# Performance work log

Hardware: AMD Instinct MI355X
Metric: run time of the kernel (lower is better)

The kernel has to match this reference:

```python
import jax, jax.numpy as jnp
import numpy as np

N_NODES = 10000
N_EDGES = 160000
HID = 128
N_LAYERS = 6
N_RBF = 50
CUTOFF = 10.0
EDGE_IN = 2 * HID + N_RBF + 1  # 307


def setup_inputs() -> dict:
    key = jax.random.key(0)
    ks = jax.random.split(key, 24)
    s = 0.05
    inp = {
        'atomic_numbers': jax.random.randint(ks[0], (N_NODES,), 0, 100),
        'coords': jax.random.normal(ks[1], (N_NODES, 3), jnp.float32),
        'edge_index': jax.random.randint(ks[2], (2, N_EDGES), 0, N_NODES),
        'embed': jax.random.normal(ks[3], (100, HID), jnp.float32) * s,
        # message_net (stacked over layers)
        'mw1': jax.random.normal(ks[4], (N_LAYERS, EDGE_IN, HID), jnp.float32) * s,
        'mb1': jnp.zeros((N_LAYERS, HID), jnp.float32),
        'mw2': jax.random.normal(ks[5], (N_LAYERS, HID, HID), jnp.float32) * s,
        'mb2': jnp.zeros((N_LAYERS, HID), jnp.float32),
        # coord_net
        'cw1': jax.random.normal(ks[6], (N_LAYERS, HID, HID), jnp.float32) * s,
        'cb1': jnp.zeros((N_LAYERS, HID), jnp.float32),
        'cw2': jax.random.normal(ks[7], (N_LAYERS, HID, 1), jnp.float32) * s,
        'cb2': jnp.zeros((N_LAYERS, 1), jnp.float32),
        # feature_net
        'fw': jax.random.normal(ks[8], (N_LAYERS, 2 * HID, HID), jnp.float32) * s,
        'fb': jnp.zeros((N_LAYERS, HID), jnp.float32),
        # energy_predictor
        'ew1': jax.random.normal(ks[9], (HID, HID), jnp.float32) * s,
        'eb1': jnp.zeros((HID,), jnp.float32),
        'ew2': jax.random.normal(ks[10], (HID, 1), jnp.float32) * s,
        'eb2': jnp.zeros((1,), jnp.float32),
    }
    return inp


def _forward(atomic_numbers, coords, edge_index, embed,
             mw1, mb1, mw2, mb2, cw1, cb1, cw2, cb2, fw, fb,
             ew1, eb1, ew2, eb2):
    silu = jax.nn.silu
    n = coords.shape[0]
    row, col = edge_index[0], edge_index[1]
    feats = embed[atomic_numbers]                    # [N, H]
    # RBF edge attributes (computed once from initial coords)
    d = jnp.linalg.norm(coords[row] - coords[col], axis=-1)[:, None]  # [E,1]
    centers = jnp.linspace(0.0, CUTOFF, N_RBF)
    width = CUTOFF / N_RBF
    rbf = jnp.exp(-((d - centers) ** 2) / width)
    cut = 0.5 * (jnp.cos(jnp.pi * d / CUTOFF) + 1.0) * (d < CUTOFF).astype(d.dtype)
    edge_attr = rbf * cut                            # [E, 50]
    for l in range(N_LAYERS):
        diff = coords[row] - coords[col]             # [E, 3]
        edist = jnp.sum(diff * diff, axis=-1, keepdims=True)  # squared dist, [E,1]
        ef = jnp.concatenate([feats[row], feats[col], edist, edge_attr], axis=-1)
        m = silu(silu(ef @ mw1[l] + mb1[l]) @ mw2[l] + mb2[l])        # [E, H]
        w = silu(m @ cw1[l] + cb1[l]) @ cw2[l] + cb2[l]               # [E, 1]
        coords = coords.at[row].add(w * diff)                         # equivariant coord update
        agg = jax.ops.segment_sum(m, row, num_segments=n)             # [N, H]
        feats = silu(jnp.concatenate([feats, agg], axis=-1) @ fw[l] + fb[l])
    atom_e = silu(feats @ ew1 + eb1) @ ew2 + eb2     # [N, 1]
    return jnp.sum(atom_e)


def reference(atomic_numbers, coords, edge_index, embed,
              mw1, mb1, mw2, mb2, cw1, cb1, cw2, cb2, fw, fb,
              ew1, eb1, ew2, eb2):
    return _forward(atomic_numbers, coords, edge_index, embed,
                    mw1, mb1, mw2, mb2, cw1, cb1, cw2, cb2, fw, fb,
                    ew1, eb1, ew2, eb2)
```

## Files before the change

kernel.cpp:

```cpp
#include <hip/hip_runtime.h>
#include <math.h>

#define N_NODES  10000
#define N_EDGES  160000
#define HID      128
#define N_LAYERS 6
#define N_RBF    50
#define EDGE_IN  307
#define KP1      320

typedef short bf16x8 __attribute__((ext_vector_type(8)));
typedef float f32x4  __attribute__((ext_vector_type(4)));

__device__ __forceinline__ float silu_f(float x) {
    return x / (1.0f + __expf(-x));
}
__device__ __forceinline__ short f2bf(float f) {
    union { float f; unsigned u; } v; v.f = f;
    unsigned r = v.u + 0x7FFFu + ((v.u >> 16) & 1u);
    return (short)(r >> 16);
}
__device__ __forceinline__ float bf2f(unsigned short s) {
    union { float f; unsigned u; } v; v.u = ((unsigned)s) << 16;
    return v.f;
}


__global__ void init_feats_kernel(const int* __restrict__ an,
                                  const float* __restrict__ embed,
                                  short* __restrict__ featsB) {
    int idx = blockIdx.x * blockDim.x + threadIdx.x;
    if (idx < N_NODES * HID) {
        int i = idx >> 7, j = idx & 127;
        featsB[idx] = f2bf(embed[an[i] * HID + j]);
    }
}

__global__ void hist_kernel(const int* __restrict__ row, int* __restrict__ cnt) {
    int e = blockIdx.x * blockDim.x + threadIdx.x;
    if (e < N_EDGES) atomicAdd(&cnt[row[e]], 1);
}

__global__ void scan_kernel(const int* __restrict__ cnt, int* __restrict__ cursor) {
    __shared__ int buf[256];
    __shared__ int carry;
    int tid = threadIdx.x;
    if (tid == 0) carry = 0;
    __syncthreads();
    for (int base = 0; base < N_NODES; base += 256) {
        int v = (base + tid < N_NODES) ? cnt[base + tid] : 0;
        buf[tid] = v;
        __syncthreads();
        for (int off = 1; off < 256; off <<= 1) {
            int x = (tid >= off) ? buf[tid - off] : 0;
            __syncthreads();
            buf[tid] += x;
            __syncthreads();
        }
        int excl = buf[tid] - v + carry;
        if (base + tid < N_NODES) cursor[base + tid] = excl;
        int tot = buf[255];
        __syncthreads();
        if (tid == 0) carry += tot;
        __syncthreads();
    }
}

__global__ void scatter_kernel(const int* __restrict__ row, int* __restrict__ cursor,
                               int* __restrict__ sorted) {
    int e = blockIdx.x * blockDim.x + threadIdx.x;
    if (e < N_EDGES) {
        int p = atomicAdd(&cursor[row[e]], 1);
        sorted[p] = e;
    }
}

__global__ void edgegeom_kernel(const int* __restrict__ sorted,
                                const int* __restrict__ erow, const int* __restrict__ ecol,
                                const float* __restrict__ coords,
                                float* __restrict__ d0, float* __restrict__ cut0) {
    int p = blockIdx.x * 256 + threadIdx.x;
    if (p < N_EDGES) {
        int e = sorted[p];
        int r = erow[e], c = ecol[e];
        float dx = coords[3*r]   - coords[3*c];
        float dy = coords[3*r+1] - coords[3*c+1];
        float dz = coords[3*r+2] - coords[3*c+2];
        float d = sqrtf(dx*dx + dy*dy + dz*dz);
        d0[p] = d;
        cut0[p] = (d < 10.0f) ? 0.5f * (__cosf(0.31415926535f * d) + 1.0f) : 0.0f;
    }
}

#define WT_L (40960 + 16384 + 16384 + 32768)
__global__ void wtrans_kernel(const float* __restrict__ mw1, const float* __restrict__ mw2,
                              const float* __restrict__ cw1, const float* __restrict__ fw,
                              short* __restrict__ wtm1, short* __restrict__ wtm2,
                              short* __restrict__ wtc1, short* __restrict__ wtf) {
    int idx = blockIdx.x * blockDim.x + threadIdx.x;
    if (idx >= N_LAYERS * WT_L) return;
    int l = idx / WT_L;
    int r = idx - l * WT_L;
    if (r < 40960) {
        int n = r / KP1, k = r - n * KP1;
        float v = (k < EDGE_IN) ? mw1[(size_t)l * EDGE_IN * HID + (size_t)k * HID + n] : 0.f;
        wtm1[(size_t)l * 40960 + r] = f2bf(v);
    } else if ((r -= 40960) < 16384) {
        int n = r >> 7, k = r & 127;
        wtm2[(size_t)l * 16384 + r] = f2bf(mw2[(size_t)l * HID * HID + (size_t)k * HID + n]);
    } else if ((r -= 16384) < 16384) {
        int n = r >> 7, k = r & 127;
        wtc1[(size_t)l * 16384 + r] = f2bf(cw1[(size_t)l * HID * HID + (size_t)k * HID + n]);
    } else {
        r -= 16384;
        int n = r >> 8, k = r & 255;
        wtf[(size_t)l * 32768 + r] = f2bf(fw[(size_t)l * 2 * HID * HID + (size_t)k * HID + n]);
    }
}


__global__ __launch_bounds__(256) void edge_kernel(
    const int* __restrict__ sorted,
    const int* __restrict__ erow, const int* __restrict__ ecol,
    const float* __restrict__ coords, float* __restrict__ coords_next,
    const short* __restrict__ featsB,
    const float* __restrict__ d0g, const float* __restrict__ cut0g,
    const short* __restrict__ wtm1, const float* __restrict__ mb1,
    const short* __restrict__ wtm2, const float* __restrict__ mb2,
    const short* __restrict__ wtc1, const float* __restrict__ cb1,
    const float* __restrict__ cw2, const float* __restrict__ cb2,
    float* __restrict__ agg)
{
    __shared__ short sA[64][72];
    __shared__ short sH[64][136];
    __shared__ int   srow[64];
    __shared__ int   scol[64];
    __shared__ float sdiff[64][3];
    __shared__ float sdist[64], sd0[64], scut[64], sW[64];
    __shared__ float sB1[HID], sB2[HID], sC1[HID], sV[HID];

    const int tid = threadIdx.x;
    const int p0 = blockIdx.x * 64;
    const int wave = tid >> 6, lane = tid & 63, quad = lane >> 4, lm = lane & 15;

    if (tid < 64) {
        int e = sorted[p0 + tid];
        int r = erow[e], c = ecol[e];
        srow[tid] = r; scol[tid] = c;
        float dx = coords[3*r]   - coords[3*c];
        float dy = coords[3*r+1] - coords[3*c+1];
        float dz = coords[3*r+2] - coords[3*c+2];
        sdiff[tid][0] = dx; sdiff[tid][1] = dy; sdiff[tid][2] = dz;
        sdist[tid] = dx*dx + dy*dy + dz*dz;
        sd0[tid]  = d0g[p0 + tid];
        scut[tid] = cut0g[p0 + tid];
    }
    if (tid < HID) {
        sB1[tid] = mb1[tid]; sB2[tid] = mb2[tid];
        sC1[tid] = cb1[tid]; sV[tid]  = cw2[tid];
    }
    __syncthreads();

    f32x4 acc[4][2];
    #pragma unroll
    for (int mt = 0; mt < 4; ++mt) { acc[mt][0] = (f32x4)0.f; acc[mt][1] = (f32x4)0.f; }

    for (int c = 0; c < 5; ++c) {
        int k0 = c * 64;
        {
            int el = tid >> 2, kq = (tid & 3) * 16;
            if (c < 4) {
                int node = (c < 2) ? srow[el] : scol[el];
                int off = (k0 & 127) + kq;
                const bf16x8* src = (const bf16x8*)&featsB[(size_t)node * HID + off];
                *(bf16x8*)&sA[el][kq]     = src[0];
                *(bf16x8*)&sA[el][kq + 8] = src[1];
            } else {
                float dv = sd0[el], ct = scut[el], ds2 = sdist[el];
                #pragma unroll
                for (int j = 0; j < 16; ++j) {
                    int k = 256 + kq + j;
                    float v = 0.f;
                    if (k == 256) v = ds2;
                    else if (k < EDGE_IN) {
                        float cen = (float)(k - 257) * (10.0f / 49.0f);
                        float t = dv - cen;
                        v = __expf(-t * t * 5.0f) * ct;
                    }
                    sA[el][kq + j] = f2bf(v);
                }
            }
        }
        __syncthreads();
        #pragma unroll
        for (int h = 0; h < 2; ++h) {
            bf16x8 af[4];
            #pragma unroll
            for (int mt = 0; mt < 4; ++mt)
                af[mt] = *(bf16x8*)&sA[mt * 16 + lm][h * 32 + quad * 8];
            #pragma unroll
            for (int nb = 0; nb < 2; ++nb) {
                int col = wave * 32 + nb * 16 + lm;
                bf16x8 bf = *(const bf16x8*)&wtm1[(size_t)col * KP1 + k0 + h * 32 + quad * 8];
                #pragma unroll
                for (int mt = 0; mt < 4; ++mt)
                    acc[mt][nb] = __builtin_amdgcn_mfma_f32_16x16x32_bf16(af[mt], bf, acc[mt][nb], 0, 0, 0);
            }
        }
        __syncthreads();
    }
    #pragma unroll
    for (int nb = 0; nb < 2; ++nb) {
        int col = wave * 32 + nb * 16 + lm;
        float b = sB1[col];
        #pragma unroll
        for (int mt = 0; mt < 4; ++mt) {
            #pragma unroll
            for (int r = 0; r < 4; ++r)
                sH[mt * 16 + quad * 4 + r][col] = f2bf(silu_f(acc[mt][nb][r] + b));
            acc[mt][nb] = (f32x4)0.f;
        }
    }
    __syncthreads();

    #pragma unroll
    for (int ks = 0; ks < 4; ++ks) {
        bf16x8 af[4];
        #pragma unroll
        for (int mt = 0; mt < 4; ++mt)
            af[mt] = *(bf16x8*)&sH[mt * 16 + lm][ks * 32 + quad * 8];
        #pragma unroll
        for (int nb = 0; nb < 2; ++nb) {
            int col = wave * 32 + nb * 16 + lm;
            bf16x8 bf = *(const bf16x8*)&wtm2[(size_t)col * HID + ks * 32 + quad * 8];
            #pragma unroll
            for (int mt = 0; mt < 4; ++mt)
                acc[mt][nb] = __builtin_amdgcn_mfma_f32_16x16x32_bf16(af[mt], bf, acc[mt][nb], 0, 0, 0);
        }
    }
    __syncthreads();
    #pragma unroll
    for (int nb = 0; nb < 2; ++nb) {
        int col = wave * 32 + nb * 16 + lm;
        float b = sB2[col];
        #pragma unroll
        for (int mt = 0; mt < 4; ++mt) {
            float g = 0.f;
            #pragma unroll
            for (int r = 0; r < 4; ++r) {
                int row = mt * 16 + quad * 4 + r;
                float mv = silu_f(acc[mt][nb][r] + b);
                sH[row][col] = f2bf(mv);
                g += mv;
                if (r == 3 || srow[row + 1] != srow[row]) {
                    atomicAdd(&agg[(size_t)srow[row] * HID + col], g);
                    g = 0.f;
                }
            }
            acc[mt][nb] = (f32x4)0.f;
        }
    }
    __syncthreads();

    #pragma unroll
    for (int ks = 0; ks < 4; ++ks) {
        bf16x8 af[4];
        #pragma unroll
        for (int mt = 0; mt < 4; ++mt)
            af[mt] = *(bf16x8*)&sH[mt * 16 + lm][ks * 32 + quad * 8];
        #pragma unroll
        for (int nb = 0; nb < 2; ++nb) {
            int col = wave * 32 + nb * 16 + lm;
            bf16x8 bf = *(const bf16x8*)&wtc1[(size_t)col * HID + ks * 32 + quad * 8];
            #pragma unroll
            for (int mt = 0; mt < 4; ++mt)
                acc[mt][nb] = __builtin_amdgcn_mfma_f32_16x16x32_bf16(af[mt], bf, acc[mt][nb], 0, 0, 0);
        }
    }
    __syncthreads();
    #pragma unroll
    for (int nb = 0; nb < 2; ++nb) {
        int col = wave * 32 + nb * 16 + lm;
        float b = sC1[col];
        #pragma unroll
        for (int mt = 0; mt < 4; ++mt)
            #pragma unroll
            for (int r = 0; r < 4; ++r)
                sH[mt * 16 + quad * 4 + r][col] = f2bf(silu_f(acc[mt][nb][r] + b));
    }
    __syncthreads();

    if (tid < 64) {
        float s = cb2[0];
        for (int k = 0; k < HID; k++) s += bf2f(((unsigned short*)sH[tid])[k]) * sV[k];
        sW[tid] = s;
    }
    __syncthreads();
    if (tid < 64) {
        bool leader = (tid == 0) || (srow[tid] != srow[tid - 1]);
        if (leader) {
            int rr = srow[tid];
            float ax = 0.f, ay = 0.f, az = 0.f;
            for (int k = tid; k < 64 && srow[k] == rr; ++k) {
                ax += sW[k] * sdiff[k][0];
                ay += sW[k] * sdiff[k][1];
                az += sW[k] * sdiff[k][2];
            }
            atomicAdd(&coords_next[3*rr+0], ax);
            atomicAdd(&coords_next[3*rr+1], ay);
            atomicAdd(&coords_next[3*rr+2], az);
        }
    }
}

__global__ __launch_bounds__(256) void node_kernel(
    const short* __restrict__ featsB, const float* __restrict__ agg,
    const short* __restrict__ wtf, const float* __restrict__ fb,
    short* __restrict__ outB)
{
    __shared__ short sA[32][72];
    __shared__ short sO[32][136];
    __shared__ float sFb[HID];

    const int tid = threadIdx.x;
    const int n0 = blockIdx.x * 32;
    const int wave = tid >> 6, lane = tid & 63, quad = lane >> 4, lm = lane & 15;

    if (tid < HID) sFb[tid] = fb[tid];

    f32x4 acc[2][2];
    acc[0][0] = (f32x4)0.f; acc[0][1] = (f32x4)0.f;
    acc[1][0] = (f32x4)0.f; acc[1][1] = (f32x4)0.f;
    __syncthreads();

    for (int c = 0; c < 4; ++c) {
        int k0 = c * 64;
        {
            int el = tid >> 3, kq = (tid & 7) * 8;
            int node = n0 + el;
            if (node < N_NODES) {
                if (c < 2) {
                    *(bf16x8*)&sA[el][kq] =
                        *(const bf16x8*)&featsB[(size_t)node * HID + k0 + kq];
                } else {
                    const float* ap = &agg[(size_t)node * HID + (k0 - 128) + kq];
                    bf16x8 v;
                    #pragma unroll
                    for (int j = 0; j < 8; ++j) v[j] = f2bf(ap[j]);
                    *(bf16x8*)&sA[el][kq] = v;
                }
            } else {
                *(bf16x8*)&sA[el][kq] = (bf16x8)0;
            }
        }
        __syncthreads();
        #pragma unroll
        for (int h = 0; h < 2; ++h) {
            bf16x8 af[2];
            af[0] = *(bf16x8*)&sA[lm][h * 32 + quad * 8];
            af[1] = *(bf16x8*)&sA[16 + lm][h * 32 + quad * 8];
            #pragma unroll
            for (int nb = 0; nb < 2; ++nb) {
                int col = wave * 32 + nb * 16 + lm;
                bf16x8 bf = *(const bf16x8*)&wtf[(size_t)col * 256 + k0 + h * 32 + quad * 8];
                acc[0][nb] = __builtin_amdgcn_mfma_f32_16x16x32_bf16(af[0], bf, acc[0][nb], 0, 0, 0);
                acc[1][nb] = __builtin_amdgcn_mfma_f32_16x16x32_bf16(af[1], bf, acc[1][nb], 0, 0, 0);
            }
        }
        __syncthreads();
    }
    #pragma unroll
    for (int nb = 0; nb < 2; ++nb) {
        int col = wave * 32 + nb * 16 + lm;
        float b = sFb[col];
        #pragma unroll
        for (int mt = 0; mt < 2; ++mt)
            #pragma unroll
            for (int r = 0; r < 4; ++r)
                sO[mt * 16 + quad * 4 + r][col] = f2bf(silu_f(acc[mt][nb][r] + b));
    }
    __syncthreads();
    {
        int row = tid >> 3, ch = (tid & 7) * 8;
        int hrow = row >> 1;
        (void)hrow;
        int node = n0 + row;
        if (node < N_NODES)
            *(bf16x8*)&outB[(size_t)node * HID + ch] = *(bf16x8*)&sO[row][ch];
        row += 0;
        if (node < N_NODES)
            *(bf16x8*)&outB[(size_t)node * HID + 64 + ch] = *(bf16x8*)&sO[row][64 + ch];
    }
}

#define FMA8(r, aq) \
    acc[r][0] += (aq)*b0.x; acc[r][1] += (aq)*b0.y; acc[r][2] += (aq)*b0.z; acc[r][3] += (aq)*b0.w; \
    acc[r][4] += (aq)*b1.x; acc[r][5] += (aq)*b1.y; acc[r][6] += (aq)*b1.z; acc[r][7] += (aq)*b1.w;

__global__ __launch_bounds__(256) void energy_kernel(
    const short* __restrict__ featsB,
    const float* __restrict__ ew1, const float* __restrict__ eb1,
    const float* __restrict__ ew2, const float* __restrict__ eb2,
    float* __restrict__ out)
{
    __shared__ float sA[64][20];
    __shared__ float sB[16][HID];
    __shared__ float sV[HID];
    __shared__ float red[256];
    int tid = threadIdx.x;
    int n0 = blockIdx.x * 64;
    const int tr = tid >> 4, tc = tid & 15;
    const int r0 = tr * 4, c0 = tc * 4, c1 = c0 + 64;
    const int el = tid >> 2, kq = (tid & 3) * 4;

    if (tid < HID) sV[tid] = ew2[tid];

    float acc[4][8];
    #pragma unroll
    for (int i = 0; i < 4; i++)
        #pragma unroll
        for (int j = 0; j < 8; j++) acc[i][j] = 0.f;

    for (int kt = 0; kt < 8; ++kt) {
        int k0 = kt * 16;
        {
            int k = k0 + kq;
            int node = n0 + el;
            float4 v = make_float4(0,0,0,0);
            if (node < N_NODES) {
                const unsigned short* p = (const unsigned short*)&featsB[(size_t)node * HID + k];
                v.x = bf2f(p[0]); v.y = bf2f(p[1]); v.z = bf2f(p[2]); v.w = bf2f(p[3]);
            }
            *(float4*)&sA[el][kq] = v;
        }
        {
            int bk = tid >> 4, bj = (tid & 15) * 8;
            int k = k0 + bk;
            *(float4*)&sB[bk][bj]     = *(const float4*)&ew1[(size_t)k * HID + bj];
            *(float4*)&sB[bk][bj + 4] = *(const float4*)&ew1[(size_t)k * HID + bj + 4];
        }
        __syncthreads();
        #pragma unroll
        for (int kk4 = 0; kk4 < 4; ++kk4) {
            float4 a0 = *(const float4*)&sA[r0 + 0][kk4 * 4];
            float4 a1 = *(const float4*)&sA[r0 + 1][kk4 * 4];
            float4 a2 = *(const float4*)&sA[r0 + 2][kk4 * 4];
            float4 a3 = *(const float4*)&sA[r0 + 3][kk4 * 4];
            #pragma unroll
            for (int q = 0; q < 4; ++q) {
                int kk = kk4 * 4 + q;
                float4 b0 = *(const float4*)&sB[kk][c0];
                float4 b1 = *(const float4*)&sB[kk][c1];
                float q0 = ((const float*)&a0)[q], q1 = ((const float*)&a1)[q];
                float q2 = ((const float*)&a2)[q], q3 = ((const float*)&a3)[q];
                FMA8(0, q0) FMA8(1, q1) FMA8(2, q2) FMA8(3, q3)
            }
        }
        __syncthreads();
    }
    float part = 0.f;
    #pragma unroll
    for (int i = 0; i < 4; i++) {
        int node = n0 + r0 + i;
        if (node < N_NODES) {
            #pragma unroll
            for (int j = 0; j < 4; j++) {
                part += silu_f(acc[i][j]     + eb1[c0+j]) * sV[c0+j];
                part += silu_f(acc[i][4 + j] + eb1[c1+j]) * sV[c1+j];
            }
        }
    }
    red[tid] = part;
    __syncthreads();
    for (int s = 128; s > 0; s >>= 1) {
        if (tid < s) red[tid] += red[tid + s];
        __syncthreads();
    }
    if (tid == 0) {
        float v = red[0];
        if (blockIdx.x == 0) v += eb2[0] * (float)N_NODES;
        atomicAdd(out, v);
    }
}


extern "C" void kernel_launch(void* const* d_in, const int* in_sizes, int n_in,
                              void* d_out, int out_size, void* d_ws, size_t ws_size,
                              hipStream_t stream)
{
    const int*   an     = (const int*)  d_in[0];
    const float* coords = (const float*)d_in[1];
    const int*   ei     = (const int*)  d_in[2];
    const float* embed  = (const float*)d_in[3];
    const float* mw1 = (const float*)d_in[4];
    const float* mb1 = (const float*)d_in[5];
    const float* mw2 = (const float*)d_in[6];
    const float* mb2 = (const float*)d_in[7];
    const float* cw1 = (const float*)d_in[8];
    const float* cb1 = (const float*)d_in[9];
    const float* cw2 = (const float*)d_in[10];
    const float* cb2 = (const float*)d_in[11];
    const float* fw  = (const float*)d_in[12];
    const float* fb  = (const float*)d_in[13];
    const float* ew1 = (const float*)d_in[14];
    const float* eb1 = (const float*)d_in[15];
    const float* ew2 = (const float*)d_in[16];
    const float* eb2 = (const float*)d_in[17];
    float* out = (float*)d_out;

    char* w = (char*)d_ws;
    size_t off = 0;
    auto alloc = [&](size_t bytes) -> char* {
        char* p = w + off;
        off = (off + bytes + 511) & ~(size_t)511;
        return p;
    };
    short* featsB0 = (short*)alloc((size_t)N_NODES * HID * 2);
    short* featsB1 = (short*)alloc((size_t)N_NODES * HID * 2);
    float* agg     = (float*)alloc((size_t)N_NODES * HID * 4);
    float* cA      = (float*)alloc((size_t)N_NODES * 3 * 4);
    float* cB      = (float*)alloc((size_t)N_NODES * 3 * 4);
    float* d0      = (float*)alloc((size_t)N_EDGES * 4);
    float* cut0    = (float*)alloc((size_t)N_EDGES * 4);
    int*   sorted  = (int*)  alloc((size_t)N_EDGES * 4);
    int*   cnt     = (int*)  alloc((size_t)N_NODES * 4);
    int*   cursor  = (int*)  alloc((size_t)N_NODES * 4);
    short* wtm1    = (short*)alloc((size_t)N_LAYERS * 40960 * 2);
    short* wtm2    = (short*)alloc((size_t)N_LAYERS * 16384 * 2);
    short* wtc1    = (short*)alloc((size_t)N_LAYERS * 16384 * 2);
    short* wtf     = (short*)alloc((size_t)N_LAYERS * 32768 * 2);

    const int* erow = ei;
    const int* ecol = ei + N_EDGES;

    hipMemsetAsync(cnt, 0, (size_t)N_NODES * 4, stream);
    init_feats_kernel<<<(N_NODES * HID + 255) / 256, 256, 0, stream>>>(an, embed, featsB0);
    wtrans_kernel<<<(N_LAYERS * WT_L + 255) / 256, 256, 0, stream>>>(
        mw1, mw2, cw1, fw, wtm1, wtm2, wtc1, wtf);
    hipMemcpyAsync(cA, coords, (size_t)N_NODES * 3 * 4, hipMemcpyDeviceToDevice, stream);
    hist_kernel<<<(N_EDGES + 255) / 256, 256, 0, stream>>>(erow, cnt);
    scan_kernel<<<1, 256, 0, stream>>>(cnt, cursor);
    scatter_kernel<<<(N_EDGES + 255) / 256, 256, 0, stream>>>(erow, cursor, sorted);
    edgegeom_kernel<<<N_EDGES / 256, 256, 0, stream>>>(sorted, erow, ecol, cA, d0, cut0);

    short* fc = featsB0; short* fn = featsB1;
    float* cc = cA;      float* cn = cB;
    for (int l = 0; l < N_LAYERS; ++l) {
        hipMemsetAsync(agg, 0, (size_t)N_NODES * HID * 4, stream);
        hipMemcpyAsync(cn, cc, (size_t)N_NODES * 3 * 4, hipMemcpyDeviceToDevice, stream);
        edge_kernel<<<N_EDGES / 64, 256, 0, stream>>>(
            sorted, erow, ecol, cc, cn, fc, d0, cut0,
            wtm1 + (size_t)l * 40960, mb1 + (size_t)l * HID,
            wtm2 + (size_t)l * 16384, mb2 + (size_t)l * HID,
            wtc1 + (size_t)l * 16384, cb1 + (size_t)l * HID,
            cw2 + (size_t)l * HID,    cb2 + l, agg);
        node_kernel<<<(N_NODES + 31) / 32, 256, 0, stream>>>(
            fc, agg, wtf + (size_t)l * 32768, fb + (size_t)l * HID, fn);
        { short* t = fc; fc = fn; fn = t; }
        { float* t = cc; cc = cn; cn = t; }
    }
    hipMemsetAsync(out, 0, 4, stream);
    energy_kernel<<<(N_NODES + 63) / 64, 256, 0, stream>>>(fc, ew1, eb1, ew2, eb2, out);
}
```

Baseline: 802.2 us.

## Make edge kernel persistent with register-resident weights and double-buffered gathers

The edge kernel becomes persistent: 512 blocks loop over 64-edge tiles and load all per-layer MFMA B-fragments (mw1, mw2, cw1) into registers once per block instead of once per tile. The feature gather for the next K-chunk is prefetched into registers and written to a second shared buffer while MFMAs run on the current one. The coord-net output layer is folded into the accumulator epilogue with shuffle reductions, which removes an sH round trip and a serial 128-wide dot product per edge. The trade-off is 36 bf16x8 weight registers per thread, which raises register pressure under launch_bounds(256,2), and a fixed grid size that may not match the number of CUs.

```diff
diff --git a/kernel.cpp b/kernel.cpp
--- a/kernel.cpp
+++ b/kernel.cpp
@@ -8,6 +8,8 @@
 #define N_RBF    50
 #define EDGE_IN  307
 #define KP1      320
+#define N_TILES  (N_EDGES / 64)
+#define EDGE_GRID 512
 
 typedef short bf16x8 __attribute__((ext_vector_type(8)));
 typedef float f32x4  __attribute__((ext_vector_type(4)));
@@ -119,7 +121,7 @@
 }
 
 
-__global__ __launch_bounds__(256) void edge_kernel(
+__global__ __launch_bounds__(256, 2) void edge_kernel(
     const int* __restrict__ sorted,
     const int* __restrict__ erow, const int* __restrict__ ecol,
     const float* __restrict__ coords, float* __restrict__ coords_next,
@@ -131,54 +133,85 @@
     const float* __restrict__ cw2, const float* __restrict__ cb2,
     float* __restrict__ agg)
 {
-    __shared__ short sA[64][72];
+    __shared__ short sA[2][64][72];
     __shared__ short sH[64][136];
     __shared__ int   srow[64];
     __shared__ int   scol[64];
     __shared__ float sdiff[64][3];
     __shared__ float sdist[64], sd0[64], scut[64], sW[64];
+    __shared__ float sWp[64][4];
     __shared__ float sB1[HID], sB2[HID], sC1[HID], sV[HID];
 
     const int tid = threadIdx.x;
-    const int p0 = blockIdx.x * 64;
     const int wave = tid >> 6, lane = tid & 63, quad = lane >> 4, lm = lane & 15;
-
-    if (tid < 64) {
-        int e = sorted[p0 + tid];
-        int r = erow[e], c = ecol[e];
-        srow[tid] = r; scol[tid] = c;
-        float dx = coords[3*r]   - coords[3*c];
-        float dy = coords[3*r+1] - coords[3*c+1];
-        float dz = coords[3*r+2] - coords[3*c+2];
-        sdiff[tid][0] = dx; sdiff[tid][1] = dy; sdiff[tid][2] = dz;
-        sdist[tid] = dx*dx + dy*dy + dz*dz;
-        sd0[tid]  = d0g[p0 + tid];
-        scut[tid] = cut0g[p0 + tid];
-    }
+    const int el = tid >> 2, kq = (tid & 3) * 16;
+    const int colA = wave * 32 + lm;
+    const int colB = colA + 16;
+
     if (tid < HID) {
         sB1[tid] = mb1[tid]; sB2[tid] = mb2[tid];
         sC1[tid] = cb1[tid]; sV[tid]  = cw2[tid];
     }
-    __syncthreads();
-
-    f32x4 acc[4][2];
+    bf16x8 bw1[20], bw2[8], bw3[8];
     #pragma unroll
-    for (int mt = 0; mt < 4; ++mt) { acc[mt][0] = (f32x4)0.f; acc[mt][1] = (f32x4)0.f; }
-
-    for (int c = 0; c < 5; ++c) {
-        int k0 = c * 64;
+    for (int c = 0; c < 5; ++c)
+        #pragma unroll
+        for (int h = 0; h < 2; ++h) {
+            bw1[c*4 + h*2 + 0] = *(const bf16x8*)&wtm1[(size_t)colA * KP1 + c*64 + h*32 + quad*8];
+            bw1[c*4 + h*2 + 1] = *(const bf16x8*)&wtm1[(size_t)colB * KP1 + c*64 + h*32 + quad*8];
+        }
+    #pragma unroll
+    for (int ks = 0; ks < 4; ++ks) {
+        bw2[ks*2 + 0] = *(const bf16x8*)&wtm2[(size_t)colA * HID + ks*32 + quad*8];
+        bw2[ks*2 + 1] = *(const bf16x8*)&wtm2[(size_t)colB * HID + ks*32 + quad*8];
+        bw3[ks*2 + 0] = *(const bf16x8*)&wtc1[(size_t)colA * HID + ks*32 + quad*8];
+        bw3[ks*2 + 1] = *(const bf16x8*)&wtc1[(size_t)colB * HID + ks*32 + quad*8];
+    }
+    const float cb2v = cb2[0];
+
+    for (int tile = blockIdx.x; tile < N_TILES; tile += EDGE_GRID) {
+        const int p0 = tile * 64;
+        __syncthreads();
+
+        if (tid < 64) {
+            int e = sorted[p0 + tid];
+            int r = erow[e], c = ecol[e];
+            srow[tid] = r; scol[tid] = c;
+            float dx = coords[3*r]   - coords[3*c];
+            float dy = coords[3*r+1] - coords[3*c+1];
+            float dz = coords[3*r+2] - coords[3*c+2];
+            sdiff[tid][0] = dx; sdiff[tid][1] = dy; sdiff[tid][2] = dz;
+            sdist[tid] = dx*dx + dy*dy + dz*dz;
+            sd0[tid]  = d0g[p0 + tid];
+            scut[tid] = cut0g[p0 + tid];
+        }
+        __syncthreads();
+
+        f32x4 acc[4][2];
+        #pragma unroll
+        for (int mt = 0; mt < 4; ++mt) { acc[mt][0] = (f32x4)0.f; acc[mt][1] = (f32x4)0.f; }
+
+        bf16x8 pA0, pA1;
         {
-            int el = tid >> 2, kq = (tid & 3) * 16;
-            if (c < 4) {
-                int node = (c < 2) ? srow[el] : scol[el];
-                int off = (k0 & 127) + kq;
-                const bf16x8* src = (const bf16x8*)&featsB[(size_t)node * HID + off];
-                *(bf16x8*)&sA[el][kq]     = src[0];
-                *(bf16x8*)&sA[el][kq + 8] = src[1];
-            } else {
+            int node = srow[el];
+            const bf16x8* src = (const bf16x8*)&featsB[(size_t)node * HID + kq];
+            pA0 = src[0]; pA1 = src[1];
+        }
+        *(bf16x8*)&sA[0][el][kq]     = pA0;
+        *(bf16x8*)&sA[0][el][kq + 8] = pA1;
+        __syncthreads();
+
+        #pragma unroll
+        for (int c = 0; c < 5; ++c) {
+            if (c < 3) {
+                int node = (c + 1 < 2) ? srow[el] : scol[el];
+                const bf16x8* src =
+                    (const bf16x8*)&featsB[(size_t)node * HID + ((c + 1) & 1) * 64 + kq];
+                pA0 = src[0]; pA1 = src[1];
+            } else if (c == 3) {
                 float dv = sd0[el], ct = scut[el], ds2 = sdist[el];
                 #pragma unroll
-                for (int j = 0; j < 16; ++j) {
+                for (int j = 0; j < 8; ++j) {
                     int k = 256 + kq + j;
                     float v = 0.f;
                     if (k == 256) v = ds2;
@@ -187,128 +220,147 @@
                         float t = dv - cen;
                         v = __expf(-t * t * 5.0f) * ct;
                     }
-                    sA[el][kq + j] = f2bf(v);
+                    pA0[j] = f2bf(v);
                 }
-            }
-        }
-        __syncthreads();
-        #pragma unroll
-        for (int h = 0; h < 2; ++h) {
+                #pragma unroll
+                for (int j = 0; j < 8; ++j) {
+                    int k = 264 + kq + j;
+                    float v = 0.f;
+                    if (k < EDGE_IN) {
+                        float cen = (float)(k - 257) * (10.0f / 49.0f);
+                        float t = dv - cen;
+                        v = __expf(-t * t * 5.0f) * ct;
+                    }
+                    pA1[j] = f2bf(v);
+                }
+            }
+            #pragma unroll
+            for (int h = 0; h < 2; ++h) {
+                bf16x8 af[4];
+                #pragma unroll
+                for (int mt = 0; mt < 4; ++mt)
+                    af[mt] = *(bf16x8*)&sA[c & 1][mt * 16 + lm][h * 32 + quad * 8];
+                #pragma unroll
+                for (int nb = 0; nb < 2; ++nb)
+                    #pragma unroll
+                    for (int mt = 0; mt < 4; ++mt)
+                        acc[mt][nb] = __builtin_amdgcn_mfma_f32_16x16x32_bf16(
+                            af[mt], bw1[c*4 + h*2 + nb], acc[mt][nb], 0, 0, 0);
+            }
+            if (c < 4) {
+                *(bf16x8*)&sA[(c + 1) & 1][el][kq]     = pA0;
+                *(bf16x8*)&sA[(c + 1) & 1][el][kq + 8] = pA1;
+            }
+            __syncthreads();
+        }
+        #pragma unroll
+        for (int nb = 0; nb < 2; ++nb) {
+            int col = wave * 32 + nb * 16 + lm;
+            float b = sB1[col];
+            #pragma unroll
+            for (int mt = 0; mt < 4; ++mt) {
+                #pragma unroll
+                for (int r = 0; r < 4; ++r)
+                    sH[mt * 16 + quad * 4 + r][col] = f2bf(silu_f(acc[mt][nb][r] + b));
+                acc[mt][nb] = (f32x4)0.f;
+            }
+        }
+        __syncthreads();
+
+        #pragma unroll
+        for (int ks = 0; ks < 4; ++ks) {
             bf16x8 af[4];
             #pragma unroll
             for (int mt = 0; mt < 4; ++mt)
-                af[mt] = *(bf16x8*)&sA[mt * 16 + lm][h * 32 + quad * 8];
+                af[mt] = *(bf16x8*)&sH[mt * 16 + lm][ks * 32 + quad * 8];
+            #pragma unroll
+            for (int nb = 0; nb < 2; ++nb)
+                #pragma unroll
+                for (int mt = 0; mt < 4; ++mt)
+                    acc[mt][nb] = __builtin_amdgcn_mfma_f32_16x16x32_bf16(
+                        af[mt], bw2[ks*2 + nb], acc[mt][nb], 0, 0, 0);
+        }
+        __syncthreads();
+        #pragma unroll
+        for (int nb = 0; nb < 2; ++nb) {
+            int col = wave * 32 + nb * 16 + lm;
+            float b = sB2[col];
+            #pragma unroll
+            for (int mt = 0; mt < 4; ++mt) {
+                float g = 0.f;
+                #pragma unroll
+                for (int r = 0; r < 4; ++r) {
+                    int row = mt * 16 + quad * 4 + r;
+                    float mv = silu_f(acc[mt][nb][r] + b);
+                    sH[row][col] = f2bf(mv);
+                    g += mv;
+                    if (r == 3 || srow[row + 1] != srow[row]) {
+                        atomicAdd(&agg[(size_t)srow[row] * HID + col], g);
+                        g = 0.f;
+                    }
+                }
+                acc[mt][nb] = (f32x4)0.f;
+            }
+        }
+        __syncthreads();
+
+        #pragma unroll
+        for (int ks = 0; ks < 4; ++ks) {
+            bf16x8 af[4];
+            #pragma unroll
+            for (int mt = 0; mt < 4; ++mt)
+                af[mt] = *(bf16x8*)&sH[mt * 16 + lm][ks * 32 + quad * 8];
+            #pragma unroll
+            for (int nb = 0; nb < 2; ++nb)
+                #pragma unroll
+                for (int mt = 0; mt < 4; ++mt)
+                    acc[mt][nb] = __builtin_amdgcn_mfma_f32_16x16x32_bf16(
+                        af[mt], bw3[ks*2 + nb], acc[mt][nb], 0, 0, 0);
+        }
+        {
+            float wp[4][4];
+            #pragma unroll
+            for (int mt = 0; mt < 4; ++mt)
+                #pragma unroll
+                for (int r = 0; r < 4; ++r) wp[mt][r] = 0.f;
             #pragma unroll
             for (int nb = 0; nb < 2; ++nb) {
                 int col = wave * 32 + nb * 16 + lm;
-                bf16x8 bf = *(const bf16x8*)&wtm1[(size_t)col * KP1 + k0 + h * 32 + quad * 8];
+                float b = sC1[col], vv = sV[col];
                 #pragma unroll
                 for (int mt = 0; mt < 4; ++mt)
-                    acc[mt][nb] = __builtin_amdgcn_mfma_f32_16x16x32_bf16(af[mt], bf, acc[mt][nb], 0, 0, 0);
-            }
-        }
-        __syncthreads();
-    }
-    #pragma unroll
-    for (int nb = 0; nb < 2; ++nb) {
-        int col = wave * 32 + nb * 16 + lm;
-        float b = sB1[col];
-        #pragma unroll
-        for (int mt = 0; mt < 4; ++mt) {
-            #pragma unroll
-            for (int r = 0; r < 4; ++r)
-                sH[mt * 16 + quad * 4 + r][col] = f2bf(silu_f(acc[mt][nb][r] + b));
-            acc[mt][nb] = (f32x4)0.f;
-        }
-    }
-    __syncthreads();
-
-    #pragma unroll
-    for (int ks = 0; ks < 4; ++ks) {
-        bf16x8 af[4];
-        #pragma unroll
-        for (int mt = 0; mt < 4; ++mt)
-            af[mt] = *(bf16x8*)&sH[mt * 16 + lm][ks * 32 + quad * 8];
-        #pragma unroll
-        for (int nb = 0; nb < 2; ++nb) {
-            int col = wave * 32 + nb * 16 + lm;
-            bf16x8 bf = *(const bf16x8*)&wtm2[(size_t)col * HID + ks * 32 + quad * 8];
+                    #pragma unroll
+                    for (int r = 0; r < 4; ++r)
+                        wp[mt][r] += silu_f(acc[mt][nb][r] + b) * vv;
+            }
             #pragma unroll
             for (int mt = 0; mt < 4; ++mt)
-                acc[mt][nb] = __builtin_amdgcn_mfma_f32_16x16x32_bf16(af[mt], bf, acc[mt][nb], 0, 0, 0);
-        }
-    }
-    __syncthreads();
-    #pragma unroll
-    for (int nb = 0; nb < 2; ++nb) {
-        int col = wave * 32 + nb * 16 + lm;
-        float b = sB2[col];
-        #pragma unroll
-        for (int mt = 0; mt < 4; ++mt) {
-            float g = 0.f;
-            #pragma unroll
-            for (int r = 0; r < 4; ++r) {
-                int row = mt * 16 + quad * 4 + r;
-                float mv = silu_f(acc[mt][nb][r] + b);
-                sH[row][col] = f2bf(mv);
-                g += mv;
-                if (r == 3 || srow[row + 1] != srow[row]) {
-                    atomicAdd(&agg[(size_t)srow[row] * HID + col], g);
-                    g = 0.f;
+                #pragma unroll
+                for (int r = 0; r < 4; ++r) {
+                    float v = wp[mt][r];
+                    v += __shfl_xor(v, 1); v += __shfl_xor(v, 2);
+                    v += __shfl_xor(v, 4); v += __shfl_xor(v, 8);
+                    if (lm == 0) sWp[mt * 16 + quad * 4 + r][wave] = v;
                 }
-            }
-            acc[mt][nb] = (f32x4)0.f;
-        }
-    }
-    __syncthreads();
-
-    #pragma unroll
-    for (int ks = 0; ks < 4; ++ks) {
-        bf16x8 af[4];
-        #pragma unroll
-        for (int mt = 0; mt < 4; ++mt)
-            af[mt] = *(bf16x8*)&sH[mt * 16 + lm][ks * 32 + quad * 8];
-        #pragma unroll
-        for (int nb = 0; nb < 2; ++nb) {
-            int col = wave * 32 + nb * 16 + lm;
-            bf16x8 bf = *(const bf16x8*)&wtc1[(size_t)col * HID + ks * 32 + quad * 8];
-            #pragma unroll
-            for (int mt = 0; mt < 4; ++mt)
-                acc[mt][nb] = __builtin_amdgcn_mfma_f32_16x16x32_bf16(af[mt], bf, acc[mt][nb], 0, 0, 0);
-        }
-    }
-    __syncthreads();
-    #pragma unroll
-    for (int nb = 0; nb < 2; ++nb) {
-        int col = wave * 32 + nb * 16 + lm;
-        float b = sC1[col];
-        #pragma unroll
-        for (int mt = 0; mt < 4; ++mt)
-            #pragma unroll
-            for (int r = 0; r < 4; ++r)
-                sH[mt * 16 + quad * 4 + r][col] = f2bf(silu_f(acc[mt][nb][r] + b));
-    }
-    __syncthreads();
-
-    if (tid < 64) {
-        float s = cb2[0];
-        for (int k = 0; k < HID; k++) s += bf2f(((unsigned short*)sH[tid])[k]) * sV[k];
-        sW[tid] = s;
-    }
-    __syncthreads();
-    if (tid < 64) {
-        bool leader = (tid == 0) || (srow[tid] != srow[tid - 1]);
-        if (leader) {
-            int rr = srow[tid];
-            float ax = 0.f, ay = 0.f, az = 0.f;
-            for (int k = tid; k < 64 && srow[k] == rr; ++k) {
-                ax += sW[k] * sdiff[k][0];
-                ay += sW[k] * sdiff[k][1];
-                az += sW[k] * sdiff[k][2];
-            }
-            atomicAdd(&coords_next[3*rr+0], ax);
-            atomicAdd(&coords_next[3*rr+1], ay);
-            atomicAdd(&coords_next[3*rr+2], az);
+        }
+        __syncthreads();
+        if (tid < 64)
+            sW[tid] = cb2v + sWp[tid][0] + sWp[tid][1] + sWp[tid][2] + sWp[tid][3];
+        __syncthreads();
+        if (tid < 64) {
+            bool leader = (tid == 0) || (srow[tid] != srow[tid - 1]);
+            if (leader) {
+                int rr = srow[tid];
+                float ax = 0.f, ay = 0.f, az = 0.f;
+                for (int k = tid; k < 64 && srow[k] == rr; ++k) {
+                    ax += sW[k] * sdiff[k][0];
+                    ay += sW[k] * sdiff[k][1];
+                    az += sW[k] * sdiff[k][2];
+                }
+                atomicAdd(&coords_next[3*rr+0], ax);
+                atomicAdd(&coords_next[3*rr+1], ay);
+                atomicAdd(&coords_next[3*rr+2], az);
+            }
         }
     }
 }
@@ -382,14 +434,11 @@
     __syncthreads();
     {
         int row = tid >> 3, ch = (tid & 7) * 8;
-        int hrow = row >> 1;
-        (void)hrow;
         int node = n0 + row;
-        if (node < N_NODES)
-            *(bf16x8*)&outB[(size_t)node * HID + ch] = *(bf16x8*)&sO[row][ch];
-        row += 0;
-        if (node < N_NODES)
+        if (node < N_NODES) {
+            *(bf16x8*)&outB[(size_t)node * HID + ch]      = *(bf16x8*)&sO[row][ch];
             *(bf16x8*)&outB[(size_t)node * HID + 64 + ch] = *(bf16x8*)&sO[row][64 + ch];
+        }
     }
 }
 
@@ -548,7 +597,7 @@
     for (int l = 0; l < N_LAYERS; ++l) {
         hipMemsetAsync(agg, 0, (size_t)N_NODES * HID * 4, stream);
         hipMemcpyAsync(cn, cc, (size_t)N_NODES * 3 * 4, hipMemcpyDeviceToDevice, stream);
-        edge_kernel<<<N_EDGES / 64, 256, 0, stream>>>(
+        edge_kernel<<<EDGE_GRID, 256, 0, stream>>>(
             sorted, erow, ecol, cc, cn, fc, d0, cut0,
             wtm1 + (size_t)l * 40960, mb1 + (size_t)l * HID,
             wtm2 + (size_t)l * 16384, mb2 + (size_t)l * HID,
```

Measured after the change: 896.7 us. 11.8% more time.
